# Kernel optimization log

Measured on AMD Instinct MI355X. Metric: run time of the kernel, lower is better.

## Reference

```python
import jax, jax.numpy as jnp
import numpy as np

D_IN = 1024
D_OUT = 1024
NUM_HEADS = 16
HEAD_DIM = D_OUT // NUM_HEADS
ORDERS = 4


def setup_inputs() -> dict:
    key = jax.random.key(0)
    k_x, k_t, k_w, k_b, k_a = jax.random.split(key, 5)
    x = jax.random.normal(k_x, (8, 4096, D_IN), dtype=jnp.float32)
    t_scalar = jax.random.uniform(k_t, (), dtype=jnp.float32)
    # Linear params (torch nn.Linear: y = x @ W.T + b)
    W = jax.random.normal(k_w, (D_OUT, D_IN), dtype=jnp.float32) * (1.0 / np.sqrt(D_IN))
    b = jax.random.normal(k_b, (D_OUT,), dtype=jnp.float32) * 0.01
    A = jax.random.normal(k_a, (NUM_HEADS, HEAD_DIM, HEAD_DIM), dtype=jnp.float32) * 0.02
    return {"x": x, "t_scalar": t_scalar, "W": W, "b": b, "A": A}


def reference(x, t_scalar, W, b, A):
    # proj_in
    z = jnp.einsum('bsd,od->bso', x, W) + b  # [B, S, d_out]
    B, S, _ = z.shape
    z = z.reshape(B, S, NUM_HEADS, HEAD_DIM)
    # Taylor series: out = sum_{k=0}^{ORDERS} (t*A)^k z / k!
    out = z
    term = z
    for order in range(1, ORDERS + 1):
        term = jnp.einsum('hij,bnhj->bnhi', A, term) * (t_scalar / float(order))
        out = out + term
    return out.reshape(B, S, D_OUT)
```

## Files before the change

### kernel.cpp

```cpp
#include <hip/hip_runtime.h>
#include <hip/hip_bf16.h>
#include <cstdint>

#define NHEAD 16
#define ORDERS 4

typedef short short8 __attribute__((ext_vector_type(8)));
typedef float f32x4 __attribute__((ext_vector_type(4)));

__device__ __forceinline__ unsigned short f32_to_bf16_rtn(float f) {
  union { float f; unsigned u; } v; v.f = f;
  unsigned r = v.u + 0x7FFFu + ((v.u >> 16) & 1u);
  return (unsigned short)(r >> 16);
}

__device__ __forceinline__ unsigned pack2(float lo, float hi) {
  __hip_bfloat162 h = __float22bfloat162_rn(float2{lo, hi});
  return *reinterpret_cast<unsigned*>(&h);
}

typedef __attribute__((address_space(1))) void gvoid;
typedef __attribute__((address_space(3))) void svoid;
__device__ __forceinline__ void gload_lds16(const void* g, void* l) {
  __builtin_amdgcn_global_load_lds((gvoid*)g, (svoid*)l, 16, 0, 0);
}

__global__ __launch_bounds__(256) void weff_kernel(
    const float* __restrict__ A, const float* __restrict__ t_ptr,
    const float* __restrict__ W, const float* __restrict__ bvec,
    unsigned short* __restrict__ Weff, float* __restrict__ beff) {
  __shared__ float Ah[64 * 65];
  __shared__ float T0[64 * 64];
  __shared__ float T1[64 * 64];

  const int tid = threadIdx.x;
  const int h = blockIdx.x >> 4;
  const int c = blockIdx.x & 15;
  const int d = tid & 63;
  const int ig = tid >> 6;

  float wreg[16];
  #pragma unroll
  for (int r = 0; r < 16; ++r)
    wreg[r] = W[(size_t)(h * 64 + ig * 16 + r) * 1024 + c * 64 + d];

  const float t = t_ptr[0];
  const int i = tid >> 2;
  const int jq = (tid & 3) << 4;

  for (int r = 0; r < 16; ++r) {
    int idx = tid + 256 * r;
    Ah[(idx >> 6) * 65 + (idx & 63)] = A[h * 4096 + idx];
  }
  float ms[16];
  #pragma unroll
  for (int cc = 0; cc < 16; ++cc) {
    float e = (i == jq + cc) ? 1.0f : 0.0f;
    T0[i * 64 + jq + cc] = e;
    ms[cc] = e;
  }
  __syncthreads();

  float* Tc = T0;
  float* Tn = T1;
  for (int k = 1; k <= ORDERS; ++k) {
    float scale = t / (float)k;
    float acc[16];
    #pragma unroll
    for (int cc = 0; cc < 16; ++cc) acc[cc] = 0.f;
    for (int l = 0; l < 64; ++l) {
      float a = Ah[i * 65 + l];
      float4 t0 = *(const float4*)&Tc[l * 64 + jq];
      float4 t1 = *(const float4*)&Tc[l * 64 + jq + 4];
      float4 t2 = *(const float4*)&Tc[l * 64 + jq + 8];
      float4 t3 = *(const float4*)&Tc[l * 64 + jq + 12];
      acc[0] += a * t0.x;  acc[1] += a * t0.y;  acc[2] += a * t0.z;  acc[3] += a * t0.w;
      acc[4] += a * t1.x;  acc[5] += a * t1.y;  acc[6] += a * t1.z;  acc[7] += a * t1.w;
      acc[8] += a * t2.x;  acc[9] += a * t2.y;  acc[10] += a * t2.z; acc[11] += a * t2.w;
      acc[12] += a * t3.x; acc[13] += a * t3.y; acc[14] += a * t3.z; acc[15] += a * t3.w;
    }
    #pragma unroll
    for (int cc = 0; cc < 16; ++cc) { acc[cc] *= scale; ms[cc] += acc[cc]; }
    #pragma unroll
    for (int u = 0; u < 4; ++u) {
      float4 v = {acc[u * 4], acc[u * 4 + 1], acc[u * 4 + 2], acc[u * 4 + 3]};
      *(float4*)&Tn[i * 64 + jq + u * 4] = v;
    }
    __syncthreads();
    float* tmp = Tc; Tc = Tn; Tn = tmp;
  }

  float* Mh = Ah;
  #pragma unroll
  for (int u = 0; u < 4; ++u) {
    float4 v = {ms[u * 4], ms[u * 4 + 1], ms[u * 4 + 2], ms[u * 4 + 3]};
    *(float4*)&Mh[i * 64 + jq + u * 4] = v;
  }
  float* Wc = T0;
  #pragma unroll
  for (int r = 0; r < 16; ++r) Wc[(ig * 16 + r) * 64 + d] = wreg[r];
  __syncthreads();

  #pragma unroll
  for (int ii = 0; ii < 16; ++ii) {
    int i2 = ig * 16 + ii;
    float acc = 0.f;
    #pragma unroll
    for (int j = 0; j < 64; ++j) acc += Mh[i2 * 64 + j] * Wc[j * 64 + d];
    Weff[(size_t)(h * 64 + i2) * 1024 + c * 64 + d] = f32_to_bf16_rtn(acc);
  }
  if (c == 0 && tid < 64) {
    float acc = 0.f;
    for (int j = 0; j < 64; ++j) acc += Mh[tid * 64 + j] * bvec[h * 64 + j];
    beff[h * 64 + tid] = acc;
  }
}

#define CSTR 132

__global__ __launch_bounds__(256, 2) void gemm_kernel(
    const float* __restrict__ X, const unsigned short* __restrict__ Wf,
    const float* __restrict__ beff, float* __restrict__ Out) {
  __shared__ __align__(16) unsigned short smem[4 * 8192];

  const int wg = blockIdx.x;
  const int swz = (wg & 7) * 256 + (wg >> 3);
  const int R = (swz >> 3) * 128;
  const int C = (swz & 7) * 128;

  const int tid = threadIdx.x;
  const int lane = tid & 63;
  const int wave = tid >> 6;
  const int wm = wave >> 1;
  const int wn = wave & 1;
  const int frow = lane & 15;
  const int fkg = lane >> 4;

  f32x4 acc[4][4];
  #pragma unroll
  for (int mi = 0; mi < 4; ++mi)
    #pragma unroll
    for (int ni = 0; ni < 4; ++ni) acc[mi][ni] = (f32x4){0.f, 0.f, 0.f, 0.f};

  const int arow = tid >> 3;
  const int aseg = tid & 7;
  const int aslot = aseg ^ (arow & 7);
  const float* Asrc = X + (size_t)(R + arow) * 1024 + aseg * 8;

  const int lr = lane >> 3;
  const int lc = lane & 7;
  const unsigned short* Bsrc = Wf + (size_t)(C + wave * 32 + lr) * 1024 + ((lc ^ lr) << 3);

  float4 aA[2][8];

  auto loadA = [&](int kt) {
    const int set = kt & 1;
    const int kb = kt * 64;
    #pragma unroll
    for (int i = 0; i < 4; ++i) {
      const float* p = Asrc + (size_t)(i * 32) * 1024 + kb;
      aA[set][2 * i] = *(const float4*)p;
      aA[set][2 * i + 1] = *(const float4*)(p + 4);
    }
  };
  auto loadB = [&](int kt) {
    unsigned short* Bd = smem + (kt & 1) * 16384 + 8192 + wave * 2048;
    const int kb = kt * 64;
    #pragma unroll
    for (int i = 0; i < 4; ++i)
      gload_lds16(Bsrc + (size_t)(i * 8) * 1024 + kb, (char*)Bd + i * 1024);
  };
  auto writeA = [&](int kt) {
    const int set = kt & 1;
    unsigned short* Ad = smem + set * 16384;
    #pragma unroll
    for (int i = 0; i < 4; ++i) {
      uint4 w = make_uint4(pack2(aA[set][2 * i].x, aA[set][2 * i].y),
                           pack2(aA[set][2 * i].z, aA[set][2 * i].w),
                           pack2(aA[set][2 * i + 1].x, aA[set][2 * i + 1].y),
                           pack2(aA[set][2 * i + 1].z, aA[set][2 * i + 1].w));
      *(uint4*)((char*)Ad + (arow + i * 32) * 128 + aslot * 16) = w;
    }
  };

  loadA(0);
  loadA(1);
  loadB(0);
  asm volatile("s_waitcnt vmcnt(12)" ::: "memory");
  __builtin_amdgcn_sched_barrier(0);

  #pragma unroll
  for (int t = 0; t < 16; ++t) {
    writeA(t);
    if (t + 2 < 16) loadA(t + 2);
    if (t + 1 < 16) loadB(t + 1);
    if (t <= 13)      asm volatile("s_waitcnt vmcnt(12)" ::: "memory");
    else if (t == 14) asm volatile("s_waitcnt vmcnt(4)" ::: "memory");
    else              asm volatile("s_waitcnt vmcnt(0)" ::: "memory");
    asm volatile("s_waitcnt lgkmcnt(0)" ::: "memory");
    __builtin_amdgcn_sched_barrier(0);
    __builtin_amdgcn_s_barrier();

    const unsigned short* As = smem + (t & 1) * 16384;
    const unsigned short* Bs = As + 8192;
    short8 afr[4][2], bfr[4][2];
    #pragma unroll
    for (int mi = 0; mi < 4; ++mi) {
      int ar = wm * 64 + mi * 16 + frow;
      #pragma unroll
      for (int kk = 0; kk < 2; ++kk) {
        int slot = (kk * 4 + fkg) ^ (ar & 7);
        afr[mi][kk] = *(const short8*)&As[ar * 64 + slot * 8];
      }
    }
    #pragma unroll
    for (int ni = 0; ni < 4; ++ni) {
      int br = wn * 64 + ni * 16 + frow;
      #pragma unroll
      for (int kk = 0; kk < 2; ++kk) {
        int slot = (kk * 4 + fkg) ^ (br & 7);
        bfr[ni][kk] = *(const short8*)&Bs[br * 64 + slot * 8];
      }
    }
    asm volatile("s_waitcnt lgkmcnt(0)" ::: "memory");
    __builtin_amdgcn_sched_barrier(0);
    __builtin_amdgcn_s_barrier();

    #pragma unroll
    for (int mi = 0; mi < 4; ++mi)
      #pragma unroll
      for (int ni = 0; ni < 4; ++ni)
        #pragma unroll
        for (int kk = 0; kk < 2; ++kk)
          acc[mi][ni] = __builtin_amdgcn_mfma_f32_16x16x32_bf16(
              afr[mi][kk], bfr[ni][kk], acc[mi][ni], 0, 0, 0);
  }
  __syncthreads();

  float* Cs = (float*)smem;
  const int c4 = (tid & 31) << 2;
  float4 bb = *(const float4*)&beff[C + c4];
  #pragma unroll
  for (int mi = 0; mi < 4; ++mi) {
    #pragma unroll
    for (int ni = 0; ni < 4; ++ni) {
      int col = wn * 64 + ni * 16 + frow;
      #pragma unroll
      for (int reg = 0; reg < 4; ++reg)
        Cs[(wm * 16 + fkg * 4 + reg) * CSTR + col] = acc[mi][ni][reg];
    }
    __syncthreads();
    #pragma unroll
    for (int it = 0; it < 4; ++it) {
      int rloc = it * 8 + (tid >> 5);
      float4 v = *(const float4*)&Cs[rloc * CSTR + c4];
      v.x += bb.x; v.y += bb.y; v.z += bb.z; v.w += bb.w;
      int grow = R + (rloc >> 4) * 64 + mi * 16 + (rloc & 15);
      *(float4*)(Out + (size_t)grow * 1024 + C + c4) = v;
    }
    __syncthreads();
  }
}

extern "C" void kernel_launch(void* const* d_in, const int* in_sizes, int n_in,
                              void* d_out, int out_size, void* d_ws, size_t ws_size,
                              hipStream_t stream) {
  const float* x = (const float*)d_in[0];
  const float* t = (const float*)d_in[1];
  const float* W = (const float*)d_in[2];
  const float* b = (const float*)d_in[3];
  const float* A = (const float*)d_in[4];
  float* out = (float*)d_out;

  char* ws = (char*)d_ws;
  unsigned short* Weff = (unsigned short*)ws;
  float* beff = (float*)(ws + (2 << 20));

  weff_kernel<<<256, 256, 0, stream>>>(A, t, W, b, Weff, beff);
  gemm_kernel<<<2048, 256, 0, stream>>>(x, Weff, beff, out);
}
```

Before: 162.7 us.

## Load A fragments directly into registers, bypassing LDS staging

The fp32 activation tile is no longer converted and written to shared memory. Each wave now loads its own A fragments straight from global memory in MFMA operand layout and packs them to bf16 in registers. Only the bf16 weight tile is still staged into LDS, which halves shared-memory use and removes the A writes and reads plus one barrier per k-step. In exchange, the two waves that share a row block both fetch the same A rows from global or cache, the loop is no longer unrolled, prefetch depth drops to one step with an explicit wait mid-iteration, and s_setprio is raised around the MFMA block.

```diff
diff --git a/kernel.cpp b/kernel.cpp
--- a/kernel.cpp
+++ b/kernel.cpp
@@ -121,7 +121,7 @@
 __global__ __launch_bounds__(256, 2) void gemm_kernel(
     const float* __restrict__ X, const unsigned short* __restrict__ Wf,
     const float* __restrict__ beff, float* __restrict__ Out) {
-  __shared__ __align__(16) unsigned short smem[4 * 8192];
+  __shared__ __align__(16) unsigned short Bs[2 * 8192];
 
   const int wg = blockIdx.x;
   const int swz = (wg & 7) * 256 + (wg >> 3);
@@ -142,90 +142,79 @@
     #pragma unroll
     for (int ni = 0; ni < 4; ++ni) acc[mi][ni] = (f32x4){0.f, 0.f, 0.f, 0.f};
 
-  const int arow = tid >> 3;
-  const int aseg = tid & 7;
-  const int aslot = aseg ^ (arow & 7);
-  const float* Asrc = X + (size_t)(R + arow) * 1024 + aseg * 8;
-
   const int lr = lane >> 3;
   const int lc = lane & 7;
-  const unsigned short* Bsrc = Wf + (size_t)(C + wave * 32 + lr) * 1024 + ((lc ^ lr) << 3);
-
-  float4 aA[2][8];
-
+  const int scol = ((lc ^ lr) << 3);
+  const unsigned short* Bsrc = Wf + (size_t)(C + wave * 32 + lr) * 1024 + scol;
+  auto stageB = [&](int kt) {
+    char* Bd = (char*)(Bs + (kt & 1) * 8192) + wave * 4096;
+    const int kb = kt * 64;
+    #pragma unroll
+    for (int i = 0; i < 4; ++i)
+      gload_lds16(Bsrc + (size_t)(i * 8) * 1024 + kb, Bd + i * 1024);
+  };
+
+  const float* Abase = X + (size_t)(R + wm * 64 + frow) * 1024 + fkg * 8;
+  float4 fA[16];
   auto loadA = [&](int kt) {
-    const int set = kt & 1;
-    const int kb = kt * 64;
-    #pragma unroll
-    for (int i = 0; i < 4; ++i) {
-      const float* p = Asrc + (size_t)(i * 32) * 1024 + kb;
-      aA[set][2 * i] = *(const float4*)p;
-      aA[set][2 * i + 1] = *(const float4*)(p + 4);
-    }
+    #pragma unroll
+    for (int mi = 0; mi < 4; ++mi)
+      #pragma unroll
+      for (int kk = 0; kk < 2; ++kk) {
+        const float* p = Abase + (size_t)(mi * 16) * 1024 + kt * 64 + kk * 32;
+        fA[(mi * 2 + kk) * 2] = *(const float4*)p;
+        fA[(mi * 2 + kk) * 2 + 1] = *(const float4*)(p + 4);
+      }
   };
-  auto loadB = [&](int kt) {
-    unsigned short* Bd = smem + (kt & 1) * 16384 + 8192 + wave * 2048;
-    const int kb = kt * 64;
-    #pragma unroll
-    for (int i = 0; i < 4; ++i)
-      gload_lds16(Bsrc + (size_t)(i * 8) * 1024 + kb, (char*)Bd + i * 1024);
+  short8 afr[4][2];
+  auto cvtA = [&]() {
+    #pragma unroll
+    for (int mi = 0; mi < 4; ++mi)
+      #pragma unroll
+      for (int kk = 0; kk < 2; ++kk) {
+        int f = (mi * 2 + kk) * 2;
+        union { unsigned u[4]; short8 s; } cv;
+        cv.u[0] = pack2(fA[f].x, fA[f].y);
+        cv.u[1] = pack2(fA[f].z, fA[f].w);
+        cv.u[2] = pack2(fA[f + 1].x, fA[f + 1].y);
+        cv.u[3] = pack2(fA[f + 1].z, fA[f + 1].w);
+        afr[mi][kk] = cv.s;
+      }
   };
-  auto writeA = [&](int kt) {
-    const int set = kt & 1;
-    unsigned short* Ad = smem + set * 16384;
-    #pragma unroll
-    for (int i = 0; i < 4; ++i) {
-      uint4 w = make_uint4(pack2(aA[set][2 * i].x, aA[set][2 * i].y),
-                           pack2(aA[set][2 * i].z, aA[set][2 * i].w),
-                           pack2(aA[set][2 * i + 1].x, aA[set][2 * i + 1].y),
-                           pack2(aA[set][2 * i + 1].z, aA[set][2 * i + 1].w));
-      *(uint4*)((char*)Ad + (arow + i * 32) * 128 + aslot * 16) = w;
-    }
-  };
 
   loadA(0);
-  loadA(1);
-  loadB(0);
-  asm volatile("s_waitcnt vmcnt(12)" ::: "memory");
+  stageB(0);
   __builtin_amdgcn_sched_barrier(0);
-
-  #pragma unroll
+  asm volatile("s_waitcnt vmcnt(4)" ::: "memory");
+  __builtin_amdgcn_sched_barrier(0);
+
   for (int t = 0; t < 16; ++t) {
-    writeA(t);
-    if (t + 2 < 16) loadA(t + 2);
-    if (t + 1 < 16) loadB(t + 1);
-    if (t <= 13)      asm volatile("s_waitcnt vmcnt(12)" ::: "memory");
-    else if (t == 14) asm volatile("s_waitcnt vmcnt(4)" ::: "memory");
-    else              asm volatile("s_waitcnt vmcnt(0)" ::: "memory");
-    asm volatile("s_waitcnt lgkmcnt(0)" ::: "memory");
+    cvtA();
+    if (t + 1 < 16) {
+      loadA(t + 1);
+      stageB(t + 1);
+    }
+    __builtin_amdgcn_sched_barrier(0);
+    if (t < 15) asm volatile("s_waitcnt vmcnt(20)" ::: "memory");
+    else        asm volatile("s_waitcnt vmcnt(0)"  ::: "memory");
     __builtin_amdgcn_sched_barrier(0);
     __builtin_amdgcn_s_barrier();
 
-    const unsigned short* As = smem + (t & 1) * 16384;
-    const unsigned short* Bs = As + 8192;
-    short8 afr[4][2], bfr[4][2];
-    #pragma unroll
-    for (int mi = 0; mi < 4; ++mi) {
-      int ar = wm * 64 + mi * 16 + frow;
-      #pragma unroll
-      for (int kk = 0; kk < 2; ++kk) {
-        int slot = (kk * 4 + fkg) ^ (ar & 7);
-        afr[mi][kk] = *(const short8*)&As[ar * 64 + slot * 8];
-      }
-    }
+    const unsigned short* B = Bs + (t & 1) * 8192;
+    short8 bfr[4][2];
     #pragma unroll
     for (int ni = 0; ni < 4; ++ni) {
       int br = wn * 64 + ni * 16 + frow;
       #pragma unroll
       for (int kk = 0; kk < 2; ++kk) {
         int slot = (kk * 4 + fkg) ^ (br & 7);
-        bfr[ni][kk] = *(const short8*)&Bs[br * 64 + slot * 8];
+        bfr[ni][kk] = *(const short8*)&B[br * 64 + slot * 8];
       }
     }
     asm volatile("s_waitcnt lgkmcnt(0)" ::: "memory");
     __builtin_amdgcn_sched_barrier(0);
-    __builtin_amdgcn_s_barrier();
-
+
+    __builtin_amdgcn_s_setprio(1);
     #pragma unroll
     for (int mi = 0; mi < 4; ++mi)
       #pragma unroll
@@ -234,10 +223,15 @@
         for (int kk = 0; kk < 2; ++kk)
           acc[mi][ni] = __builtin_amdgcn_mfma_f32_16x16x32_bf16(
               afr[mi][kk], bfr[ni][kk], acc[mi][ni], 0, 0, 0);
+    __builtin_amdgcn_s_setprio(0);
+
+    if (t + 1 < 16) asm volatile("s_waitcnt vmcnt(4)" ::: "memory");
+    __builtin_amdgcn_sched_barrier(0);
+    __builtin_amdgcn_s_barrier();
   }
   __syncthreads();
 
-  float* Cs = (float*)smem;
+  float* Cs = (float*)Bs;
   const int c4 = (tid & 31) << 2;
   float4 bb = *(const float4*)&beff[C + c4];
   #pragma unroll
```

Result: slower. 289.8 us (+78.2%).
